# Optimization experiments

Measured on AMD Instinct MI355X. Metric: run time of the kernel, lower is better.

Reference implementation:

```python
import jax, jax.numpy as jnp
import numpy as np


def setup_inputs() -> dict:
    key = jax.random.key(0)
    ks = jax.random.split(key, 12)
    b, S, c, d = 2, 20, 256, 4
    sc = 0.05

    def w(k, shape):
        return jax.random.normal(k, shape, jnp.float32) * sc

    return {
        "x": jax.random.normal(ks[0], (b, S, c, d, d), jnp.float32),
        "W1": w(ks[1], (2 * (c + 2), 256)), "b1": jnp.zeros((256,), jnp.float32),
        "W2": w(ks[2], (256, 256)), "b2": jnp.zeros((256,), jnp.float32),
        "W3": w(ks[3], (256, 256)), "b3": jnp.zeros((256,), jnp.float32),
        "W4": w(ks[4], (256, 256)), "b4": jnp.zeros((256,), jnp.float32),
        "Wf1": w(ks[5], (256, 256)), "bf1": jnp.zeros((256,), jnp.float32),
        "Wf2": w(ks[6], (256, 256)), "bf2": jnp.zeros((256,), jnp.float32),
        "Wf3": w(ks[7], (256, 29)), "bf3": jnp.zeros((29,), jnp.float32),
        "Wf4": w(ks[8], (29, 1)), "bf4": jnp.zeros((1,), jnp.float32),
    }


def reference(x, W1, b1, W2, b2, W3, b3, W4, b4,
              Wf1, bf1, Wf2, bf2, Wf3, bf3, Wf4, bf4):
    # x: [b, S, c, d, d] post-repnet features
    b, S, c, d, _ = x.shape
    cc = c + 2  # feature channels after coord concat
    # coord[0,i,j] = i/d, coord[1,i,j] = j/d (matches torch transpose chain)
    r = jnp.arange(d, dtype=x.dtype) / d
    coord = jnp.stack(jnp.meshgrid(r, r, indexing="ij"), axis=0)  # [2, d, d]
    xc = jnp.concatenate(
        [x, jnp.broadcast_to(coord, (b, S, 2, d, d))], axis=2)     # [b,S,cc,d,d]
    xf = xc.reshape(b, S, cc, d * d).transpose(0, 1, 3, 2)         # [b,S,P,cc]

    # First g layer on concat([x_i, x_j]) == split W1 and broadcast-add.
    # Pair feature at (b, s1, s2, p1, p2) = [x[b,s2,:,p2], x[b,s1,:,p1]].
    A = jnp.einsum("bspc,ch->bsph", xf, W1[:cc])   # x_i contribution
    B = jnp.einsum("bspc,ch->bsph", xf, W1[cc:])   # x_j contribution
    h = jax.nn.relu(A[:, None, :, None, :, :] + B[:, :, None, :, None, :] + b1)
    # h: [b, S, S, P, P, 256]
    h = jax.nn.relu(h @ W2 + b2)
    h = jax.nn.relu(h @ W3 + b3)
    h = jax.nn.relu(h @ W4 + b4)
    pooled = h.sum(axis=(3, 4))                    # [b, S, S, 256]

    y = jax.nn.relu(pooled @ Wf1 + bf1)
    y = jax.nn.relu(y @ Wf2 + bf2)  # Dropout is identity in eval/reference
    y = jax.nn.relu(y @ Wf3 + bf3)
    score = jax.nn.sigmoid(y @ Wf4 + bf4)[..., 0]  # [b, S, S]
    return score
```

## Files before the change

### kernel.cpp

```cpp
#include <hip/hip_runtime.h>
#include <hip/hip_bf16.h>
#include <math.h>

typedef _Float16 f16x8 __attribute__((ext_vector_type(8)));
typedef _Float16 f16x4 __attribute__((ext_vector_type(4)));
typedef float f32x4 __attribute__((ext_vector_type(4)));

#define LDH 264

__global__ void prep_ab(const float* __restrict__ x, const float* __restrict__ W1,
                        const float* __restrict__ b1,
                        float* __restrict__ A, float* __restrict__ B) {
    int blk = blockIdx.x;
    int bs = blk >> 2, pg = blk & 3;
    __shared__ float xs[258 * 4];
    for (int i = threadIdx.x; i < 1024; i += 512) {
        int c = i >> 2, pp = i & 3;
        xs[i] = x[bs * 4096 + c * 16 + pg * 4 + pp];
    }
    if (threadIdx.x < 8) {
        int pp = threadIdx.x & 3, c = 256 + (threadIdx.x >> 2);
        int p = pg * 4 + pp;
        xs[c * 4 + pp] = (float)((c == 256) ? (p >> 2) : (p & 3)) * 0.25f;
    }
    __syncthreads();
    int half = threadIdx.x >> 8;
    int col  = threadIdx.x & 255;
    float acc[4] = {0.f, 0.f, 0.f, 0.f};
    const float* Wp = W1 + half * 258 * 256 + col;
    for (int c = 0; c < 258; c++) {
        float w = Wp[c * 256];
#pragma unroll
        for (int pp = 0; pp < 4; pp++) acc[pp] += xs[c * 4 + pp] * w;
    }
    float* out = half ? B : A;
    float bias = half ? 0.f : b1[col];
#pragma unroll
    for (int pp = 0; pp < 4; pp++)
        out[(bs * 16 + pg * 4 + pp) * 256 + col] = acc[pp] + bias;
}

__global__ void prep_w(const float* __restrict__ W2, const float* __restrict__ W3,
                       const float* __restrict__ W4, _Float16* __restrict__ Wt) {
    int blk = blockIdx.x;
    int t   = threadIdx.x;
    int kk = blk & 7, cg = (blk >> 3) & 15, L = blk >> 7;
    int l = t >> 3, e = t & 7;
    int col = cg * 16 + (l & 15);
    int k   = kk * 32 + (l >> 4) * 8 + e;
    const float* W = (L == 0) ? W2 : (L == 1) ? W3 : W4;
    Wt[blk * 512 + t] = (_Float16)W[k * 256 + col];
}

__global__ __launch_bounds__(512, 4) void pairnet(
        const float* __restrict__ A, const float* __restrict__ B,
        const _Float16* __restrict__ Wt,
        const float* __restrict__ b2, const float* __restrict__ b3,
        const float* __restrict__ b4, float* __restrict__ pooled4) {
    __shared__ _Float16 hb[128 * LDH];

    int blk  = blockIdx.x;
    int half = blk & 1;
    int bss  = blk >> 1;
    int s2   = bss % 20;
    int s1   = (bss / 20) % 20;
    int b    = bss / 400;
    int tid  = threadIdx.x;

    const float* Abase = A + (b * 20 + s2) * 16 * 256;
    const float* Bbase = B + ((b * 20 + s1) * 16 + half * 8) * 256;
#pragma unroll
    for (int it = 0; it < 8; it++) {
        int u = it * 512 + tid;
        int r = u >> 5;
        int c = (u & 31) * 8;
        const float* Ap = Abase + (r & 15) * 256 + c;
        const float* Bp = Bbase + (r >> 4) * 256 + c;
        float4 a0 = *(const float4*)(Ap);
        float4 a1 = *(const float4*)(Ap + 4);
        float4 b0 = *(const float4*)(Bp);
        float4 b1 = *(const float4*)(Bp + 4);
        f16x8 hv;
        hv[0] = (_Float16)fmaxf(a0.x + b0.x, 0.f);
        hv[1] = (_Float16)fmaxf(a0.y + b0.y, 0.f);
        hv[2] = (_Float16)fmaxf(a0.z + b0.z, 0.f);
        hv[3] = (_Float16)fmaxf(a0.w + b0.w, 0.f);
        hv[4] = (_Float16)fmaxf(a1.x + b1.x, 0.f);
        hv[5] = (_Float16)fmaxf(a1.y + b1.y, 0.f);
        hv[6] = (_Float16)fmaxf(a1.z + b1.z, 0.f);
        hv[7] = (_Float16)fmaxf(a1.w + b1.w, 0.f);
        *(f16x8*)(hb + r * LDH + c) = hv;
    }
    __syncthreads();

    int wid = tid >> 6, lane = tid & 63;
    int row0 = (wid >> 2) * 64;
    int col0 = (wid & 3) * 64;
    int lr = lane & 15, lk = lane >> 4;

#pragma unroll
    for (int L = 0; L < 3; L++) {
        const float* bias = (L == 0) ? b2 : (L == 1) ? b3 : b4;
        const _Float16* wb = Wt + (size_t)((L * 16 + (wid & 3) * 4) * 8) * 512 + lane * 8;

        f32x4 acc[4][4];
#pragma unroll
        for (int m = 0; m < 4; m++)
#pragma unroll
            for (int n = 0; n < 4; n++) acc[m][n] = (f32x4){0.f, 0.f, 0.f, 0.f};

#pragma unroll
        for (int kk = 0; kk < 8; kk++) {
            f16x8 w[4], a[4];
#pragma unroll
            for (int n = 0; n < 4; n++)
                w[n] = *(const f16x8*)(wb + (n * 8 + kk) * 512);
#pragma unroll
            for (int m = 0; m < 4; m++)
                a[m] = *(const f16x8*)(hb + (row0 + 16 * m + lr) * LDH + kk * 32 + 8 * lk);
#pragma unroll
            for (int m = 0; m < 4; m++)
#pragma unroll
                for (int n = 0; n < 4; n++)
                    acc[m][n] = __builtin_amdgcn_mfma_f32_16x16x32_f16(
                        w[n], a[m], acc[m][n], 0, 0, 0);
        }

        if (L < 2) {
            __syncthreads();
#pragma unroll
            for (int n = 0; n < 4; n++) {
                int cb = col0 + 16 * n + 4 * lk;
                float4 b4v = *(const float4*)(bias + cb);
#pragma unroll
                for (int m = 0; m < 4; m++) {
                    int row = row0 + 16 * m + lr;
                    f16x4 hv;
                    hv[0] = (_Float16)fmaxf(acc[m][n][0] + b4v.x, 0.f);
                    hv[1] = (_Float16)fmaxf(acc[m][n][1] + b4v.y, 0.f);
                    hv[2] = (_Float16)fmaxf(acc[m][n][2] + b4v.z, 0.f);
                    hv[3] = (_Float16)fmaxf(acc[m][n][3] + b4v.w, 0.f);
                    *(f16x4*)(hb + row * LDH + cb) = hv;
                }
            }
            __syncthreads();
        } else {
#pragma unroll
            for (int n = 0; n < 4; n++) {
                int cb = col0 + 16 * n + 4 * lk;
                float4 b4v = *(const float4*)(bias + cb);
                f32x4 s = (f32x4){0.f, 0.f, 0.f, 0.f};
#pragma unroll
                for (int m = 0; m < 4; m++) {
                    s[0] += fmaxf(acc[m][n][0] + b4v.x, 0.f);
                    s[1] += fmaxf(acc[m][n][1] + b4v.y, 0.f);
                    s[2] += fmaxf(acc[m][n][2] + b4v.z, 0.f);
                    s[3] += fmaxf(acc[m][n][3] + b4v.w, 0.f);
                }
#pragma unroll
                for (int mask = 1; mask <= 8; mask <<= 1) {
#pragma unroll
                    for (int c = 0; c < 4; c++) s[c] += __shfl_xor(s[c], mask);
                }
                if (lr == 0) {
                    int slab = half * 2 + (wid >> 2);
                    float4 sv; sv.x = s[0]; sv.y = s[1]; sv.z = s[2]; sv.w = s[3];
                    *(float4*)(pooled4 + ((size_t)slab * 800 + bss) * 256 + cb) = sv;
                }
            }
        }
    }
}

__global__ void final_mlp(const float* __restrict__ pooled4,
        const float* __restrict__ Wf1, const float* __restrict__ bf1,
        const float* __restrict__ Wf2, const float* __restrict__ bf2,
        const float* __restrict__ Wf3, const float* __restrict__ bf3,
        const float* __restrict__ Wf4, const float* __restrict__ bf4,
        float* __restrict__ out) {
    __shared__ float p[4][256], y[4][256], z[4][256], y3[4][29];
    int r0 = blockIdx.x * 4;
    int t  = threadIdx.x;
    for (int i = t; i < 1024; i += 256) {
        int r = i >> 8, c = i & 255;
        float v = 0.f;
#pragma unroll
        for (int q = 0; q < 4; q++)
            v += pooled4[((size_t)q * 800 + r0 + r) * 256 + c];
        p[r][c] = v;
    }
    __syncthreads();
    float acc[4];
#pragma unroll
    for (int r = 0; r < 4; r++) acc[r] = bf1[t];
    for (int k = 0; k < 256; k++) {
        float w = Wf1[k * 256 + t];
#pragma unroll
        for (int r = 0; r < 4; r++) acc[r] += p[r][k] * w;
    }
#pragma unroll
    for (int r = 0; r < 4; r++) y[r][t] = fmaxf(acc[r], 0.f);
    __syncthreads();
#pragma unroll
    for (int r = 0; r < 4; r++) acc[r] = bf2[t];
    for (int k = 0; k < 256; k++) {
        float w = Wf2[k * 256 + t];
#pragma unroll
        for (int r = 0; r < 4; r++) acc[r] += y[r][k] * w;
    }
#pragma unroll
    for (int r = 0; r < 4; r++) z[r][t] = fmaxf(acc[r], 0.f);
    __syncthreads();
    if (t < 116) {
        int r = t / 29, c = t % 29;
        float a = bf3[c];
        for (int k = 0; k < 256; k++) a += z[r][k] * Wf3[k * 29 + c];
        y3[r][c] = fmaxf(a, 0.f);
    }
    __syncthreads();
    if (t < 4) {
        float zz = bf4[0];
#pragma unroll
        for (int c = 0; c < 29; c++) zz += y3[t][c] * Wf4[c];
        out[r0 + t] = 1.f / (1.f + expf(-zz));
    }
}

extern "C" void kernel_launch(void* const* d_in, const int* in_sizes, int n_in,
                              void* d_out, int out_size, void* d_ws, size_t ws_size,
                              hipStream_t stream) {
    const float* x   = (const float*)d_in[0];
    const float* W1  = (const float*)d_in[1];
    const float* b1  = (const float*)d_in[2];
    const float* W2  = (const float*)d_in[3];
    const float* b2  = (const float*)d_in[4];
    const float* W3  = (const float*)d_in[5];
    const float* b3  = (const float*)d_in[6];
    const float* W4  = (const float*)d_in[7];
    const float* b4  = (const float*)d_in[8];
    const float* Wf1 = (const float*)d_in[9];
    const float* bf1 = (const float*)d_in[10];
    const float* Wf2 = (const float*)d_in[11];
    const float* bf2 = (const float*)d_in[12];
    const float* Wf3 = (const float*)d_in[13];
    const float* bf3 = (const float*)d_in[14];
    const float* Wf4 = (const float*)d_in[15];
    const float* bf4 = (const float*)d_in[16];

    float* A       = (float*)d_ws;
    float* B       = A + 640 * 256;
    float* pooled4 = B + 640 * 256;
    _Float16* Wt   = (_Float16*)(pooled4 + 4 * 800 * 256);

    prep_ab<<<160, 512, 0, stream>>>(x, W1, b1, A, B);
    prep_w<<<384, 512, 0, stream>>>(W2, W3, W4, Wt);
    pairnet<<<1600, 512, 0, stream>>>(A, B, Wt, b2, b3, b4, pooled4);
    final_mlp<<<200, 256, 0, stream>>>(pooled4, Wf1, bf1, Wf2, bf2, Wf3, bf3, Wf4, bf4,
                                       (float*)d_out);
}
```

Before: 124.6 us.

## Merge prep kernels, split pairnet into quarter blocks, batch weight loads

Fuses the two prep kernels into a single launch to cut launch overhead. Splits each pairnet block into 4 blocks of 256 threads handling 64 rows, which halves LDS per block and raises block count for occupancy, but each block now re-reads all weight tiles for fewer rows. The prep and final MLP loops now load 8 weights at a time so that loads can be issued ahead of the FMAs.

```diff
diff --git a/kernel.cpp b/kernel.cpp
--- a/kernel.cpp
+++ b/kernel.cpp
@@ -8,12 +8,25 @@
 
 #define LDH 264
 
-__global__ void prep_ab(const float* __restrict__ x, const float* __restrict__ W1,
-                        const float* __restrict__ b1,
-                        float* __restrict__ A, float* __restrict__ B) {
-    int blk = blockIdx.x;
+__global__ void prep(const float* __restrict__ x, const float* __restrict__ W1,
+                     const float* __restrict__ b1,
+                     const float* __restrict__ W2, const float* __restrict__ W3,
+                     const float* __restrict__ W4,
+                     float* __restrict__ A, float* __restrict__ B,
+                     _Float16* __restrict__ Wt) {
+    __shared__ float xs[258 * 4];
+    if (blockIdx.x < 384) {
+        int blk = blockIdx.x, t = threadIdx.x;
+        int kk = blk & 7, cg = (blk >> 3) & 15, L = blk >> 7;
+        int l = t >> 3, e = t & 7;
+        int col = cg * 16 + (l & 15);
+        int k   = kk * 32 + (l >> 4) * 8 + e;
+        const float* W = (L == 0) ? W2 : (L == 1) ? W3 : W4;
+        Wt[blk * 512 + t] = (_Float16)W[k * 256 + col];
+        return;
+    }
+    int blk = blockIdx.x - 384;
     int bs = blk >> 2, pg = blk & 3;
-    __shared__ float xs[258 * 4];
     for (int i = threadIdx.x; i < 1024; i += 512) {
         int c = i >> 2, pp = i & 3;
         xs[i] = x[bs * 4096 + c * 16 + pg * 4 + pp];
@@ -28,7 +41,18 @@
     int col  = threadIdx.x & 255;
     float acc[4] = {0.f, 0.f, 0.f, 0.f};
     const float* Wp = W1 + half * 258 * 256 + col;
-    for (int c = 0; c < 258; c++) {
+#pragma unroll 1
+    for (int c0 = 0; c0 < 256; c0 += 8) {
+        float w[8];
+#pragma unroll
+        for (int j = 0; j < 8; j++) w[j] = Wp[(c0 + j) * 256];
+#pragma unroll
+        for (int j = 0; j < 8; j++)
+#pragma unroll
+            for (int pp = 0; pp < 4; pp++) acc[pp] += xs[(c0 + j) * 4 + pp] * w[j];
+    }
+#pragma unroll
+    for (int c = 256; c < 258; c++) {
         float w = Wp[c * 256];
 #pragma unroll
         for (int pp = 0; pp < 4; pp++) acc[pp] += xs[c * 4 + pp] * w;
@@ -40,38 +64,26 @@
         out[(bs * 16 + pg * 4 + pp) * 256 + col] = acc[pp] + bias;
 }
 
-__global__ void prep_w(const float* __restrict__ W2, const float* __restrict__ W3,
-                       const float* __restrict__ W4, _Float16* __restrict__ Wt) {
-    int blk = blockIdx.x;
-    int t   = threadIdx.x;
-    int kk = blk & 7, cg = (blk >> 3) & 15, L = blk >> 7;
-    int l = t >> 3, e = t & 7;
-    int col = cg * 16 + (l & 15);
-    int k   = kk * 32 + (l >> 4) * 8 + e;
-    const float* W = (L == 0) ? W2 : (L == 1) ? W3 : W4;
-    Wt[blk * 512 + t] = (_Float16)W[k * 256 + col];
-}
-
-__global__ __launch_bounds__(512, 4) void pairnet(
+__global__ __launch_bounds__(256, 4) void pairnet(
         const float* __restrict__ A, const float* __restrict__ B,
         const _Float16* __restrict__ Wt,
         const float* __restrict__ b2, const float* __restrict__ b3,
         const float* __restrict__ b4, float* __restrict__ pooled4) {
-    __shared__ _Float16 hb[128 * LDH];
-
-    int blk  = blockIdx.x;
-    int half = blk & 1;
-    int bss  = blk >> 1;
-    int s2   = bss % 20;
-    int s1   = (bss / 20) % 20;
-    int b    = bss / 400;
-    int tid  = threadIdx.x;
+    __shared__ _Float16 hb[64 * LDH];
+
+    int blk = blockIdx.x;
+    int qtr = blk & 3;
+    int bss = blk >> 2;
+    int s2  = bss % 20;
+    int s1  = (bss / 20) % 20;
+    int b   = bss / 400;
+    int tid = threadIdx.x;
 
     const float* Abase = A + (b * 20 + s2) * 16 * 256;
-    const float* Bbase = B + ((b * 20 + s1) * 16 + half * 8) * 256;
+    const float* Bbase = B + ((b * 20 + s1) * 16 + qtr * 4) * 256;
 #pragma unroll
     for (int it = 0; it < 8; it++) {
-        int u = it * 512 + tid;
+        int u = it * 256 + tid;
         int r = u >> 5;
         int c = (u & 31) * 8;
         const float* Ap = Abase + (r & 15) * 256 + c;
@@ -94,14 +106,13 @@
     __syncthreads();
 
     int wid = tid >> 6, lane = tid & 63;
-    int row0 = (wid >> 2) * 64;
-    int col0 = (wid & 3) * 64;
+    int col0 = wid * 64;
     int lr = lane & 15, lk = lane >> 4;
 
 #pragma unroll
     for (int L = 0; L < 3; L++) {
         const float* bias = (L == 0) ? b2 : (L == 1) ? b3 : b4;
-        const _Float16* wb = Wt + (size_t)((L * 16 + (wid & 3) * 4) * 8) * 512 + lane * 8;
+        const _Float16* wb = Wt + (size_t)((L * 16 + wid * 4) * 8) * 512 + lane * 8;
 
         f32x4 acc[4][4];
 #pragma unroll
@@ -117,7 +128,7 @@
                 w[n] = *(const f16x8*)(wb + (n * 8 + kk) * 512);
 #pragma unroll
             for (int m = 0; m < 4; m++)
-                a[m] = *(const f16x8*)(hb + (row0 + 16 * m + lr) * LDH + kk * 32 + 8 * lk);
+                a[m] = *(const f16x8*)(hb + (16 * m + lr) * LDH + kk * 32 + 8 * lk);
 #pragma unroll
             for (int m = 0; m < 4; m++)
 #pragma unroll
@@ -134,7 +145,7 @@
                 float4 b4v = *(const float4*)(bias + cb);
 #pragma unroll
                 for (int m = 0; m < 4; m++) {
-                    int row = row0 + 16 * m + lr;
+                    int row = 16 * m + lr;
                     f16x4 hv;
                     hv[0] = (_Float16)fmaxf(acc[m][n][0] + b4v.x, 0.f);
                     hv[1] = (_Float16)fmaxf(acc[m][n][1] + b4v.y, 0.f);
@@ -163,9 +174,8 @@
                     for (int c = 0; c < 4; c++) s[c] += __shfl_xor(s[c], mask);
                 }
                 if (lr == 0) {
-                    int slab = half * 2 + (wid >> 2);
                     float4 sv; sv.x = s[0]; sv.y = s[1]; sv.z = s[2]; sv.w = s[3];
-                    *(float4*)(pooled4 + ((size_t)slab * 800 + bss) * 256 + cb) = sv;
+                    *(float4*)(pooled4 + ((size_t)qtr * 800 + bss) * 256 + cb) = sv;
                 }
             }
         }
@@ -193,20 +203,30 @@
     float acc[4];
 #pragma unroll
     for (int r = 0; r < 4; r++) acc[r] = bf1[t];
-    for (int k = 0; k < 256; k++) {
-        float w = Wf1[k * 256 + t];
-#pragma unroll
-        for (int r = 0; r < 4; r++) acc[r] += p[r][k] * w;
+#pragma unroll 1
+    for (int k0 = 0; k0 < 256; k0 += 8) {
+        float w[8];
+#pragma unroll
+        for (int j = 0; j < 8; j++) w[j] = Wf1[(k0 + j) * 256 + t];
+#pragma unroll
+        for (int j = 0; j < 8; j++)
+#pragma unroll
+            for (int r = 0; r < 4; r++) acc[r] += p[r][k0 + j] * w[j];
     }
 #pragma unroll
     for (int r = 0; r < 4; r++) y[r][t] = fmaxf(acc[r], 0.f);
     __syncthreads();
 #pragma unroll
     for (int r = 0; r < 4; r++) acc[r] = bf2[t];
-    for (int k = 0; k < 256; k++) {
-        float w = Wf2[k * 256 + t];
-#pragma unroll
-        for (int r = 0; r < 4; r++) acc[r] += y[r][k] * w;
+#pragma unroll 1
+    for (int k0 = 0; k0 < 256; k0 += 8) {
+        float w[8];
+#pragma unroll
+        for (int j = 0; j < 8; j++) w[j] = Wf2[(k0 + j) * 256 + t];
+#pragma unroll
+        for (int j = 0; j < 8; j++)
+#pragma unroll
+            for (int r = 0; r < 4; r++) acc[r] += y[r][k0 + j] * w[j];
     }
 #pragma unroll
     for (int r = 0; r < 4; r++) z[r][t] = fmaxf(acc[r], 0.f);
@@ -214,7 +234,14 @@
     if (t < 116) {
         int r = t / 29, c = t % 29;
         float a = bf3[c];
-        for (int k = 0; k < 256; k++) a += z[r][k] * Wf3[k * 29 + c];
+#pragma unroll 1
+        for (int k0 = 0; k0 < 256; k0 += 8) {
+            float w[8];
+#pragma unroll
+            for (int j = 0; j < 8; j++) w[j] = Wf3[(k0 + j) * 29 + c];
+#pragma unroll
+            for (int j = 0; j < 8; j++) a += z[r][k0 + j] * w[j];
+        }
         y3[r][c] = fmaxf(a, 0.f);
     }
     __syncthreads();
@@ -252,9 +279,8 @@
     float* pooled4 = B + 640 * 256;
     _Float16* Wt   = (_Float16*)(pooled4 + 4 * 800 * 256);
 
-    prep_ab<<<160, 512, 0, stream>>>(x, W1, b1, A, B);
-    prep_w<<<384, 512, 0, stream>>>(W2, W3, W4, Wt);
-    pairnet<<<1600, 512, 0, stream>>>(A, B, Wt, b2, b3, b4, pooled4);
+    prep<<<544, 512, 0, stream>>>(x, W1, b1, W2, W3, W4, A, B, Wt);
+    pairnet<<<3200, 256, 0, stream>>>(A, B, Wt, b2, b3, b4, pooled4);
     final_mlp<<<200, 256, 0, stream>>>(pooled4, Wf1, bf1, Wf2, bf2, Wf3, bf3, Wf4, bf4,
                                        (float*)d_out);
 }
```

Result: no change. 122.5 us (-1.7%).
